# Performance work log

Hardware: AMD Instinct MI355X
Metric: run time of the kernel (lower is better)

The kernel has to match this reference:

```python
import jax, jax.numpy as jnp
import numpy as np


def setup_inputs() -> dict:
    key = jax.random.key(0)
    k1, k2 = jax.random.split(key)
    B, C, H, W = 8, 64, 128, 128
    C_w, ks = 8, 3
    x = jax.random.normal(k1, (B, C, H, W), dtype=jnp.float32)
    w = jax.random.normal(k2, (B, C_w, ks * ks, H, W), dtype=jnp.float32)
    return {"x": x, "w": w}


def _ska_2d(x, w):
    # x: (B,C,H,W); w: (B,C_w,ks^2,H,W); groups = C // C_w
    B, C, H, W = x.shape
    C_w, ks2 = w.shape[1], w.shape[2]
    ks = int(round(np.sqrt(ks2)))
    pad = ks // 2
    groups = C // C_w
    x_pad = jnp.pad(x, ((0, 0), (0, 0), (pad, pad), (pad, pad)))
    # Gather shifted views instead of materializing a giant unfold copy; order
    # matches F.unfold (kernel row-major: i outer, j inner).
    patches = jnp.stack(
        [x_pad[:, :, i:i + H, j:j + W] for i in range(ks) for j in range(ks)],
        axis=2,
    )  # (B, C, ks^2, H, W)
    # Split channels as (groups, C_w): output channel c = g*C_w + cw uses weight channel cw.
    p = patches.reshape(B, groups, C_w, ks2, H, W)
    out = jnp.einsum('bgckhw,bckhw->bgchw', p, w)  # sum over kernel positions k
    return out.reshape(B, C, H, W)


def reference(x, w):
    return _ska_2d(x, w)
```

## Files before the change

kernel.cpp:

```cpp
#include <hip/hip_runtime.h>
#include <stdint.h>


#define SKA_W 128
#define SKA_HW (128 * 128)
#define TILE_ROWS 8
#define STAGE_ROWS 10

typedef float vf4 __attribute__((ext_vector_type(4)));

__global__ __launch_bounds__(256, 4) void SKA_44830868635847_kernel(
        const float* __restrict__ x,
        const float* __restrict__ wgt,
        float* __restrict__ out) {
    __shared__ float lds[8 * STAGE_ROWS * SKA_W];

    const int t     = threadIdx.x;
    const int bid   = blockIdx.x;
    const int htile = bid & 15;
    const int cw    = (bid >> 4) & 7;
    const int b     = bid >> 7;
    const int h0    = htile * TILE_ROWS;

    const int w4 = t & 31;
    const int hl = t >> 5;
    const int h  = h0 + hl;
    const int w0 = w4 * 4;

    const float* xb = x + (size_t)(b * 64 + cw) * SKA_HW;
    const int wavebase = t & ~63;
#pragma unroll
    for (int rep = 0; rep < 10; ++rep) {
        int idx = rep * 256 + t;
        int ch  = idx / 320;
        int rem = idx - ch * 320;
        int r   = rem >> 5;
        int c4  = rem & 31;
        int xrow = h0 - 1 + r;
        xrow = xrow < 0 ? 0 : (xrow > 127 ? 127 : xrow);
        const float* gsrc = xb + (size_t)ch * 8 * SKA_HW + (size_t)xrow * SKA_W + c4 * 4;
        __builtin_amdgcn_global_load_lds(
            (const __attribute__((address_space(1))) uint32_t*)gsrc,
            (__attribute__((address_space(3))) uint32_t*)&lds[(size_t)(rep * 256 + wavebase) * 4],
            16, 0, 0);
    }

    const float* wbase = wgt + ((size_t)(b * 8 + cw) * 9) * SKA_HW + (size_t)h * SKA_W + w0;
    vf4 wv[9];
#pragma unroll
    for (int k = 0; k < 9; ++k)
        wv[k] = *(const vf4*)(wbase + (size_t)k * SKA_HW);
    if (h == 0)   { wv[0] = (vf4)(0.f); wv[1] = (vf4)(0.f); wv[2] = (vf4)(0.f); }
    if (h == 127) { wv[6] = (vf4)(0.f); wv[7] = (vf4)(0.f); wv[8] = (vf4)(0.f); }

    __syncthreads();

    const size_t obase = (size_t)(b * 64 + cw) * SKA_HW + (size_t)h * SKA_W + w0;
#pragma unroll
    for (int g = 0; g < 8; ++g) {
        vf4 acc = (vf4)(0.f);
#pragma unroll
        for (int i = 0; i < 3; ++i) {
            const float* lrow = &lds[(g * STAGE_ROWS + hl + i) * SKA_W + w0];
            vf4 mid = *(const vf4*)lrow;
            float xl  = __shfl_up(mid.w, 1);
            xl  = (w4 == 0)  ? 0.f : xl;
            float xr4 = __shfl_down(mid.x, 1);
            xr4 = (w4 == 31) ? 0.f : xr4;
            vf4 wl = wv[i * 3 + 0];
            vf4 wm = wv[i * 3 + 1];
            vf4 wr = wv[i * 3 + 2];
            acc.x += wl.x * xl    + wm.x * mid.x + wr.x * mid.y;
            acc.y += wl.y * mid.x + wm.y * mid.y + wr.y * mid.z;
            acc.z += wl.z * mid.y + wm.z * mid.z + wr.z * mid.w;
            acc.w += wl.w * mid.z + wm.w * mid.w + wr.w * xr4;
        }
        *(vf4*)(out + obase + (size_t)g * 8 * SKA_HW) = acc;
    }
}

extern "C" void kernel_launch(void* const* d_in, const int* in_sizes, int n_in,
                              void* d_out, int out_size, void* d_ws, size_t ws_size,
                              hipStream_t stream) {
    const float* x   = (const float*)d_in[0];
    const float* wgt = (const float*)d_in[1];
    float* out = (float*)d_out;

    SKA_44830868635847_kernel<<<1024, 256, 0, stream>>>(x, wgt, out);
}
```

Baseline: 103.3 us.

## Double rows per block to 16 and remap block index across XCDs

Each block now computes 16 output rows per channel group instead of 8, staging 18 input rows in LDS. This reduces halo reload overhead and halves the block count. Each thread processes two rows with separate weight register sets. The block index is permuted so adjacent launch IDs map to different batches/channels. The cost is higher LDS and register use, lower occupancy and fewer blocks for latency hiding.

New measurement: 105.7 us. 2.3% more time.

```diff
diff --git a/kernel.cpp b/kernel.cpp
--- a/kernel.cpp
+++ b/kernel.cpp
@@ -4,36 +4,37 @@
 
 #define SKA_W 128
 #define SKA_HW (128 * 128)
-#define TILE_ROWS 8
-#define STAGE_ROWS 10
+#define TILE_ROWS 16
+#define STAGE_ROWS 18
 
 typedef float vf4 __attribute__((ext_vector_type(4)));
 
-__global__ __launch_bounds__(256, 4) void SKA_44830868635847_kernel(
+__global__ __launch_bounds__(256, 2) void SKA_44830868635847_kernel(
         const float* __restrict__ x,
         const float* __restrict__ wgt,
         float* __restrict__ out) {
     __shared__ float lds[8 * STAGE_ROWS * SKA_W];
 
-    const int t     = threadIdx.x;
-    const int bid   = blockIdx.x;
-    const int htile = bid & 15;
-    const int cw    = (bid >> 4) & 7;
-    const int b     = bid >> 7;
+    const int t = threadIdx.x;
+
+    const int p = blockIdx.x;
+    const int L = (p & 7) * 64 + (p >> 3);
+    const int htile = L & 7;
+    const int cw    = (L >> 3) & 7;
+    const int b     = L >> 6;
     const int h0    = htile * TILE_ROWS;
 
     const int w4 = t & 31;
     const int hl = t >> 5;
-    const int h  = h0 + hl;
     const int w0 = w4 * 4;
 
     const float* xb = x + (size_t)(b * 64 + cw) * SKA_HW;
     const int wavebase = t & ~63;
 #pragma unroll
-    for (int rep = 0; rep < 10; ++rep) {
+    for (int rep = 0; rep < 18; ++rep) {
         int idx = rep * 256 + t;
-        int ch  = idx / 320;
-        int rem = idx - ch * 320;
+        int ch  = idx / 576;
+        int rem = idx - ch * 576;
         int r   = rem >> 5;
         int c4  = rem & 31;
         int xrow = h0 - 1 + r;
@@ -45,37 +46,60 @@
             16, 0, 0);
     }
 
-    const float* wbase = wgt + ((size_t)(b * 8 + cw) * 9) * SKA_HW + (size_t)h * SKA_W + w0;
-    vf4 wv[9];
+    const int hA = h0 + hl;
+    const int hB = hA + 8;
+    const float* wbA = wgt + ((size_t)(b * 8 + cw) * 9) * SKA_HW + (size_t)hA * SKA_W + w0;
+    vf4 wvA[9], wvB[9];
 #pragma unroll
-    for (int k = 0; k < 9; ++k)
-        wv[k] = *(const vf4*)(wbase + (size_t)k * SKA_HW);
-    if (h == 0)   { wv[0] = (vf4)(0.f); wv[1] = (vf4)(0.f); wv[2] = (vf4)(0.f); }
-    if (h == 127) { wv[6] = (vf4)(0.f); wv[7] = (vf4)(0.f); wv[8] = (vf4)(0.f); }
+    for (int k = 0; k < 9; ++k) {
+        wvA[k] = *(const vf4*)(wbA + (size_t)k * SKA_HW);
+        wvB[k] = *(const vf4*)(wbA + (size_t)k * SKA_HW + 8 * SKA_W);
+    }
+    if (hA == 0)   { wvA[0] = (vf4)(0.f); wvA[1] = (vf4)(0.f); wvA[2] = (vf4)(0.f); }
+    if (hB == 127) { wvB[6] = (vf4)(0.f); wvB[7] = (vf4)(0.f); wvB[8] = (vf4)(0.f); }
 
     __syncthreads();
 
-    const size_t obase = (size_t)(b * 64 + cw) * SKA_HW + (size_t)h * SKA_W + w0;
+    const size_t obaseA = (size_t)(b * 64 + cw) * SKA_HW + (size_t)hA * SKA_W + w0;
 #pragma unroll
     for (int g = 0; g < 8; ++g) {
-        vf4 acc = (vf4)(0.f);
+        vf4 accA = (vf4)(0.f);
+        vf4 accB = (vf4)(0.f);
 #pragma unroll
         for (int i = 0; i < 3; ++i) {
-            const float* lrow = &lds[(g * STAGE_ROWS + hl + i) * SKA_W + w0];
-            vf4 mid = *(const vf4*)lrow;
-            float xl  = __shfl_up(mid.w, 1);
-            xl  = (w4 == 0)  ? 0.f : xl;
-            float xr4 = __shfl_down(mid.x, 1);
-            xr4 = (w4 == 31) ? 0.f : xr4;
-            vf4 wl = wv[i * 3 + 0];
-            vf4 wm = wv[i * 3 + 1];
-            vf4 wr = wv[i * 3 + 2];
-            acc.x += wl.x * xl    + wm.x * mid.x + wr.x * mid.y;
-            acc.y += wl.y * mid.x + wm.y * mid.y + wr.y * mid.z;
-            acc.z += wl.z * mid.y + wm.z * mid.z + wr.z * mid.w;
-            acc.w += wl.w * mid.z + wm.w * mid.w + wr.w * xr4;
+            {
+                const float* lrow = &lds[(g * STAGE_ROWS + hl + i) * SKA_W + w0];
+                vf4 mid = *(const vf4*)lrow;
+                float xl  = __shfl_up(mid.w, 1);
+                xl  = (w4 == 0)  ? 0.f : xl;
+                float xr4 = __shfl_down(mid.x, 1);
+                xr4 = (w4 == 31) ? 0.f : xr4;
+                vf4 wl = wvA[i * 3 + 0];
+                vf4 wm = wvA[i * 3 + 1];
+                vf4 wr = wvA[i * 3 + 2];
+                accA.x += wl.x * xl    + wm.x * mid.x + wr.x * mid.y;
+                accA.y += wl.y * mid.x + wm.y * mid.y + wr.y * mid.z;
+                accA.z += wl.z * mid.y + wm.z * mid.z + wr.z * mid.w;
+                accA.w += wl.w * mid.z + wm.w * mid.w + wr.w * xr4;
+            }
+            {
+                const float* lrow = &lds[(g * STAGE_ROWS + hl + 8 + i) * SKA_W + w0];
+                vf4 mid = *(const vf4*)lrow;
+                float xl  = __shfl_up(mid.w, 1);
+                xl  = (w4 == 0)  ? 0.f : xl;
+                float xr4 = __shfl_down(mid.x, 1);
+                xr4 = (w4 == 31) ? 0.f : xr4;
+                vf4 wl = wvB[i * 3 + 0];
+                vf4 wm = wvB[i * 3 + 1];
+                vf4 wr = wvB[i * 3 + 2];
+                accB.x += wl.x * xl    + wm.x * mid.x + wr.x * mid.y;
+                accB.y += wl.y * mid.x + wm.y * mid.y + wr.y * mid.z;
+                accB.z += wl.z * mid.y + wm.z * mid.z + wr.z * mid.w;
+                accB.w += wl.w * mid.z + wm.w * mid.w + wr.w * xr4;
+            }
         }
-        *(vf4*)(out + obase + (size_t)g * 8 * SKA_HW) = acc;
+        *(vf4*)(out + obaseA + (size_t)g * 8 * SKA_HW) = accA;
+        *(vf4*)(out + obaseA + (size_t)g * 8 * SKA_HW + 8 * SKA_W) = accB;
     }
 }
 
@@ -86,5 +110,5 @@
     const float* wgt = (const float*)d_in[1];
     float* out = (float*)d_out;
 
-    SKA_44830868635847_kernel<<<1024, 256, 0, stream>>>(x, wgt, out);
+    SKA_44830868635847_kernel<<<512, 256, 0, stream>>>(x, wgt, out);
 }
```
